# Kernel optimization log

Hardware: AMD Instinct MI355X
Metric: run time of the kernel (lower is better)

The kernel has to match this reference:

```python
import jax, jax.numpy as jnp
import numpy as np
import math

FACTOR = 5

def setup_inputs() -> dict:
    key = jax.random.key(0)
    k1, k2, k3, k4 = jax.random.split(key, 4)
    B, L, H, D = 4, 2048, 8, 64
    sample_k = FACTOR * math.ceil(math.log(L))  # 40
    queries = jax.random.normal(k1, (B, L, H, D), dtype=jnp.float32)
    keys = jax.random.normal(k2, (B, L, H, D), dtype=jnp.float32)
    values = jax.random.normal(k3, (B, L, H, D), dtype=jnp.float32)
    index_sample = jax.random.randint(k4, (L, sample_k), 0, L, dtype=jnp.int32)
    return {"queries": queries, "keys": keys, "values": values, "index_sample": index_sample}

def reference(queries, keys, values, index_sample):
    B, L_Q, H, D = queries.shape
    L_K = keys.shape[1]
    # [B,L,H,D] -> [B,H,L,D]
    Q = jnp.swapaxes(queries, 1, 2)
    K = jnp.swapaxes(keys, 1, 2)
    # values are cumsum'ed along the length axis before attention
    Vc = jnp.cumsum(jnp.swapaxes(values, 1, 2), axis=-2)
    u = min(FACTOR * math.ceil(math.log(L_Q)), L_Q)  # n_top
    # --- _prob_QK ---
    # gather sampled keys per query position: [B,H,L_Q,sample_k,D]
    K_sample = K[:, :, index_sample, :]
    # sampled scores: [B,H,L_Q,sample_k]
    Q_K_sample = jnp.einsum('bhqd,bhqsd->bhqs', Q, K_sample)
    # sparsity measure M = max - mean(scaled by L_K)
    M = Q_K_sample.max(axis=-1) - Q_K_sample.sum(axis=-1) / L_K  # [B,H,L_Q]
    M_top = jax.lax.top_k(M, u)[1]  # [B,H,u] query indices
    # gather top queries: [B,H,u,D]
    Q_reduce = jnp.take_along_axis(Q, M_top[..., None], axis=2)
    # full scores for selected queries: [B,H,u,L_K]
    scores = jnp.einsum('bhud,bhkd->bhuk', Q_reduce, K)
    scale = 1.0 / math.sqrt(D)
    scores = scores * scale
    # mask_flag=False, output_attention=False -> plain softmax then matmul with cumsum'ed V
    attn = jax.nn.softmax(scores, axis=-1)
    context = jnp.einsum('bhuk,bhkd->bhud', attn, Vc)  # [B,H,u,D]
    return context
```

## Files before the change

### kernel.cpp

```cpp
#include <hip/hip_runtime.h>
#include <math.h>

#define B 4
#define L 2048
#define H 8
#define D 64
#define SK 40
#define U 40
#define JC 16
#define JCL (L / JC)
#define CSG 32

#define OFF_M     0
#define OFF_TOP   262144
#define OFF_T     270336
#define OFF_PART  10756096
#define OFF_CSUM  15998976

__device__ __forceinline__ float dot4(float4 a, float4 b) {
    return fmaf(a.x, b.x, fmaf(a.y, b.y, fmaf(a.z, b.z, a.w * b.w)));
}

__global__ __launch_bounds__(256) void k_msamp(const float* __restrict__ Q,
                                               const float* __restrict__ K,
                                               const int* __restrict__ idx,
                                               float* __restrict__ M) {
    int g  = blockIdx.x & 7;
    int b  = g >> 1;
    int hh = g & 1;
    int t  = threadIdx.x;
    int wave = t >> 6;
    int lane = t & 63;
    int qp = lane >> 5;
    int hp = (lane >> 3) & 3;
    int c  = lane & 7;
    int h  = hh * 4 + hp;
    int q  = (blockIdx.x >> 3) * 8 + wave * 2 + qp;

    const float* qrow = Q + (size_t)((b * L + q) * H + h) * D + c * 8;
    float4 qa = *(const float4*)qrow;
    float4 qb = *(const float4*)(qrow + 4);

    int s1 = lane & 31;
    int v1 = idx[q * SK + s1];
    int s2 = 32 + s1; if (s2 > SK - 1) s2 = SK - 1;
    int v2 = idx[q * SK + s2];

    const float* kbase = K + (size_t)b * L * H * D + (size_t)h * D + c * 8;

    float vmax = -__builtin_inff();
    float vsum = 0.f;
#pragma unroll 8
    for (int s = 0; s < SK; ++s) {
        int kidx = (s < 32) ? __shfl(v1, qp * 32 + s, 64)
                            : __shfl(v2, qp * 32 + (s - 32), 64);
        const float* kp = kbase + (size_t)kidx * (H * D);
        float4 ka = *(const float4*)kp;
        float4 kb = *(const float4*)(kp + 4);
        float d8 = dot4(qa, ka) + dot4(qb, kb);
        d8 += __shfl_xor(d8, 1, 64);
        d8 += __shfl_xor(d8, 2, 64);
        d8 += __shfl_xor(d8, 4, 64);
        vmax = fmaxf(vmax, d8);
        vsum += d8;
    }
    if (c == 0) M[(size_t)(b * H + h) * L + q] = vmax - vsum * (1.0f / (float)L);
}

__global__ __launch_bounds__(256) void k_topk(const float* __restrict__ M,
                                              int* __restrict__ top) {
    __shared__ unsigned long long cand[L];
    __shared__ unsigned int bins[256];
    __shared__ unsigned int red[256];
    __shared__ int cnt2;

    int bh = blockIdx.x;
    int tid = threadIdx.x;
    const float* m = M + (size_t)bh * L;

    bins[tid] = 0;
    if (tid == 0) cnt2 = 0;

    const float4* m4 = (const float4*)(m + tid * 8);
    float4 fa = m4[0], fb = m4[1];
    float f8[8] = {fa.x, fa.y, fa.z, fa.w, fb.x, fb.y, fb.z, fb.w};
    unsigned int u8[8];
    unsigned int umin = 0xFFFFFFFFu, umax = 0u;
#pragma unroll
    for (int e = 0; e < 8; ++e) {
        unsigned int bits = __float_as_uint(f8[e]);
        unsigned int u = (bits & 0x80000000u) ? ~bits : (bits | 0x80000000u);
        u8[e] = u;
        umin = min(umin, u);
        umax = max(umax, u);
    }
    red[tid] = umin;
    __syncthreads();
    for (int s = 128; s; s >>= 1) {
        if (tid < s) red[tid] = min(red[tid], red[tid + s]);
        __syncthreads();
    }
    unsigned int kmin = red[0];
    __syncthreads();
    red[tid] = umax;
    __syncthreads();
    for (int s = 128; s; s >>= 1) {
        if (tid < s) red[tid] = max(red[tid], red[tid + s]);
        __syncthreads();
    }
    unsigned int kmax = red[0];
    __syncthreads();

    unsigned int range = kmax - kmin;
    if (range == 0u) {
        if (tid < U) top[bh * U + tid] = tid;
        return;
    }
    int hb = 31 - __clz(range);
    int shift = (hb > 7) ? (hb - 7) : 0;

#pragma unroll
    for (int e = 0; e < 8; ++e) {
        unsigned int bin = (u8[e] - kmin) >> shift;
        atomicAdd(&bins[bin], 1u);
    }
    __syncthreads();

    red[tid] = bins[tid];
    __syncthreads();
    for (int s = 1; s < 256; s <<= 1) {
        unsigned int add = (tid + s < 256) ? red[tid + s] : 0u;
        __syncthreads();
        red[tid] += add;
        __syncthreads();
    }
    int cnt = __syncthreads_count(red[tid] >= U);
    unsigned int t = (unsigned int)(cnt - 1);

#pragma unroll
    for (int e = 0; e < 8; ++e) {
        unsigned int u = u8[e];
        if (((u - kmin) >> shift) >= t) {
            int pos = atomicAdd(&cnt2, 1);
            int i = tid * 8 + e;
            cand[pos] = ((unsigned long long)u << 11) | (unsigned long long)(2047 - i);
        }
    }
    __syncthreads();
    int C = cnt2;

    for (int j = tid; j < C; j += 256) {
        unsigned long long kj = cand[j];
        int r = 0;
        for (int kk = 0; kk < C; ++kk) r += (cand[kk] > kj);
        if (r < U) top[bh * U + r] = 2047 - (int)(kj & 0x7FFull);
    }
}


__global__ __launch_bounds__(512, 4) void k_phA(const float* __restrict__ Q,
                                                const float* __restrict__ K,
                                                const int* __restrict__ top,
                                                float* __restrict__ T,
                                                float* __restrict__ csum) {
    __shared__ __align__(16) float4 sQ4[U * 16];
    int tid = threadIdx.x;
    int bh = blockIdx.x >> 4;
    int kc = blockIdx.x & 15;
    int b = bh >> 3, h = bh & (H - 1);

    for (int i = tid; i < U * 16; i += 512) {
        int u = i >> 4, c = i & 15;
        int qidx = top[bh * U + u];
        sQ4[i] = *((const float4*)(Q + (size_t)((b * L + qidx) * H + h) * D) + c);
    }

    int ugrp   = tid >> 7;
    int colgrp = tid & 127;
    int col = kc * 128 + colgrp;

    const float4* kr = (const float4*)(K + (size_t)((b * L + col) * H + h) * D);
    float4 kv[16];
#pragma unroll
    for (int i = 0; i < 16; ++i) kv[i] = kr[i];
    __syncthreads();

    float* Tb = T + (size_t)bh * U * L;
    int cs = 2 * kc + (colgrp >> 6);
#pragma unroll
    for (int uu = 0; uu < 10; ++uu) {
        int u = ugrp * 10 + uu;
        float s = 0.f;
#pragma unroll
        for (int i = 0; i < 16; ++i) s += dot4(sQ4[u * 16 + i], kv[i]);
        float e = __expf(s * 0.125f);
        Tb[(size_t)u * L + col] = e;
        float c0 = e;
#pragma unroll
        for (int o = 1; o < 64; o <<= 1) c0 += __shfl_xor(c0, o, 64);
        if ((colgrp & 63) == 0) csum[((size_t)bh * U + u) * CSG + cs] = c0;
    }
}

__global__ __launch_bounds__(512, 4) void k_phB(const float* __restrict__ V,
                                                const float* __restrict__ T,
                                                const float* __restrict__ csum,
                                                float* __restrict__ part) {
    __shared__ __align__(16) float sT[U * JCL];
    int tid = threadIdx.x;
    int bh = blockIdx.x >> 4;
    int jc = blockIdx.x & 15;
    int b = bh >> 3, h = bh & (H - 1);
    int w8   = tid >> 6;
    int lane = tid & 63;

    int j2 = lane >> 4;
    int d4 = lane & 15;
    int jlane = lane & 31;

    const float* Eg = T + (size_t)bh * U * L + jc * JCL;
    for (int r = 0; r < 5; ++r) {
        int u = w8 * 5 + r;
        float cv = csum[((size_t)bh * U + u) * CSG + jlane];
        float tv = (jlane > 2 * jc + 1) ? cv : 0.f;
        tv += __shfl_xor(tv, 1, 64);
        tv += __shfl_xor(tv, 2, 64);
        tv += __shfl_xor(tv, 4, 64);
        tv += __shfl_xor(tv, 8, 64);
        tv += __shfl_xor(tv, 16, 64);
        float el = Eg[(size_t)u * L + lane];
        float eh = Eg[(size_t)u * L + 64 + lane];
        float sh = eh;
#pragma unroll
        for (int s = 1; s < 64; s <<= 1) {
            float o = __shfl_down(sh, s, 64);
            sh += (lane + s < 64) ? o : 0.f;
        }
        float th = __shfl(sh, 0, 64);
        float sl = el;
#pragma unroll
        for (int s = 1; s < 64; s <<= 1) {
            float o = __shfl_down(sl, s, 64);
            sl += (lane + s < 64) ? o : 0.f;
        }
        sT[u * JCL + lane]      = sl + th + tv;
        sT[u * JCL + 64 + lane] = sh + tv;
    }
    __syncthreads();

    float4 acc[5];
#pragma unroll
    for (int uu = 0; uu < 5; ++uu) acc[uu] = make_float4(0.f, 0.f, 0.f, 0.f);

    const float* Vb = V + (size_t)(b * L) * (H * D) + (size_t)h * D + d4 * 4;
#pragma unroll 4
    for (int it = 0; it < JCL / 4; ++it) {
        int j = it * 4 + j2;
        float4 v4 = *(const float4*)(Vb + (size_t)(jc * JCL + j) * (H * D));
#pragma unroll
        for (int uu = 0; uu < 5; ++uu) {
            float tj = sT[(w8 * 5 + uu) * JCL + j];
            acc[uu].x = fmaf(tj, v4.x, acc[uu].x);
            acc[uu].y = fmaf(tj, v4.y, acc[uu].y);
            acc[uu].z = fmaf(tj, v4.z, acc[uu].z);
            acc[uu].w = fmaf(tj, v4.w, acc[uu].w);
        }
    }

    float* po = part + ((size_t)jc * (B * H) + bh) * (U * D);
#pragma unroll
    for (int uu = 0; uu < 5; ++uu) {
        float4 a = acc[uu];
        a.x += __shfl_xor(a.x, 16, 64); a.y += __shfl_xor(a.y, 16, 64);
        a.z += __shfl_xor(a.z, 16, 64); a.w += __shfl_xor(a.w, 16, 64);
        a.x += __shfl_xor(a.x, 32, 64); a.y += __shfl_xor(a.y, 32, 64);
        a.z += __shfl_xor(a.z, 32, 64); a.w += __shfl_xor(a.w, 32, 64);
        if (j2 == 0) *(float4*)(po + (w8 * 5 + uu) * D + d4 * 4) = a;
    }
}

__global__ __launch_bounds__(256) void k_red(const float* __restrict__ part,
                                             const float* __restrict__ csum,
                                             float* __restrict__ out) {
    __shared__ float sden[4];
    int o = blockIdx.x * 256 + threadIdx.x;
    int bh = o / (U * D);
    int rest = o - bh * (U * D);
    int u = rest >> 6;
    int tid = threadIdx.x;
    int ubase = ((blockIdx.x * 256) % (U * D)) >> 6;

    if (tid < 128) {
        int ul = tid >> 5, j = tid & 31;
        float v = csum[((size_t)bh * U + ubase + ul) * CSG + j];
        v += __shfl_xor(v, 1, 64);
        v += __shfl_xor(v, 2, 64);
        v += __shfl_xor(v, 4, 64);
        v += __shfl_xor(v, 8, 64);
        v += __shfl_xor(v, 16, 64);
        if (j == 0) sden[ul] = v;
    }
    __syncthreads();

    float s = 0.f;
#pragma unroll
    for (int jc = 0; jc < JC; ++jc)
        s += part[(size_t)(jc * (B * H) + bh) * (U * D) + rest];
    out[o] = s / sden[u - ubase];
}

extern "C" void kernel_launch(void* const* d_in, const int* in_sizes, int n_in,
                              void* d_out, int out_size, void* d_ws, size_t ws_size,
                              hipStream_t stream) {
    const float* Q  = (const float*)d_in[0];
    const float* K  = (const float*)d_in[1];
    const float* V  = (const float*)d_in[2];
    const int* idx  = (const int*)d_in[3];
    float* out = (float*)d_out;

    float* M    = (float*)((char*)d_ws + OFF_M);
    int*   top  = (int*)  ((char*)d_ws + OFF_TOP);
    float* T    = (float*)((char*)d_ws + OFF_T);
    float* part = (float*)((char*)d_ws + OFF_PART);
    float* csum = (float*)((char*)d_ws + OFF_CSUM);

    k_msamp<<<(L / 8) * 8, 256, 0, stream>>>(Q, K, idx, M);
    k_topk<<<B * H, 256, 0, stream>>>(M, top);
    k_phA<<<B * H * 16, 512, 0, stream>>>(Q, K, top, T, csum);
    k_phB<<<B * H * 16, 512, 0, stream>>>(V, T, csum, part);
    k_red<<<(B * H * U * D) / 256, 256, 0, stream>>>(part, csum, out);
}
```

Before: 144.0 us.

## Fuse score and cumsum-V phases, defer cross-chunk prefix to reduction via V sums

Merges the exp-score kernel and the suffix-weighted V accumulation into one kernel, so exponentiated scores stay in shared memory and are never written to or read back from a global T buffer. The cross-chunk suffix term, which needed every chunk's csum before phase B could start, is now applied in the reduction kernel as a weighted sum of per-chunk V column sums. This removes one launch and roughly 10 MB of global traffic. In exchange it adds a vsum buffer, a segmented scan in k_red, and extra LDS use per block (sE of U*JCL floats plus sQ4), which may lower occupancy.

```diff
diff --git a/kernel.cpp b/kernel.cpp
--- a/kernel.cpp
+++ b/kernel.cpp
@@ -13,9 +13,9 @@
 
 #define OFF_M     0
 #define OFF_TOP   262144
-#define OFF_T     270336
-#define OFF_PART  10756096
-#define OFF_CSUM  15998976
+#define OFF_PART  270336
+#define OFF_CSUM  5513216
+#define OFF_VSUM  5677056
 
 __device__ __forceinline__ float dot4(float4 a, float4 b) {
     return fmaf(a.x, b.x, fmaf(a.y, b.y, fmaf(a.z, b.z, a.w * b.w)));
@@ -157,16 +157,18 @@
     }
 }
 
-
-__global__ __launch_bounds__(512, 4) void k_phA(const float* __restrict__ Q,
-                                                const float* __restrict__ K,
-                                                const int* __restrict__ top,
-                                                float* __restrict__ T,
-                                                float* __restrict__ csum) {
+__global__ __launch_bounds__(512, 4) void k_phAB(const float* __restrict__ Q,
+                                                 const float* __restrict__ K,
+                                                 const int* __restrict__ top,
+                                                 const float* __restrict__ V,
+                                                 float* __restrict__ part,
+                                                 float* __restrict__ csum,
+                                                 float* __restrict__ vsum) {
     __shared__ __align__(16) float4 sQ4[U * 16];
+    __shared__ __align__(16) float sE[U * JCL];
     int tid = threadIdx.x;
     int bh = blockIdx.x >> 4;
-    int kc = blockIdx.x & 15;
+    int jc = blockIdx.x & 15;
     int b = bh >> 3, h = bh & (H - 1);
 
     for (int i = tid; i < U * 16; i += 512) {
@@ -177,7 +179,7 @@
 
     int ugrp   = tid >> 7;
     int colgrp = tid & 127;
-    int col = kc * 128 + colgrp;
+    int col = jc * 128 + colgrp;
 
     const float4* kr = (const float4*)(K + (size_t)((b * L + col) * H + h) * D);
     float4 kv[16];
@@ -185,8 +187,7 @@
     for (int i = 0; i < 16; ++i) kv[i] = kr[i];
     __syncthreads();
 
-    float* Tb = T + (size_t)bh * U * L;
-    int cs = 2 * kc + (colgrp >> 6);
+    int cs = 2 * jc + (colgrp >> 6);
 #pragma unroll
     for (int uu = 0; uu < 10; ++uu) {
         int u = ugrp * 10 + uu;
@@ -194,42 +195,20 @@
 #pragma unroll
         for (int i = 0; i < 16; ++i) s += dot4(sQ4[u * 16 + i], kv[i]);
         float e = __expf(s * 0.125f);
-        Tb[(size_t)u * L + col] = e;
+        sE[u * JCL + colgrp] = e;
         float c0 = e;
 #pragma unroll
         for (int o = 1; o < 64; o <<= 1) c0 += __shfl_xor(c0, o, 64);
         if ((colgrp & 63) == 0) csum[((size_t)bh * U + u) * CSG + cs] = c0;
     }
-}
-
-__global__ __launch_bounds__(512, 4) void k_phB(const float* __restrict__ V,
-                                                const float* __restrict__ T,
-                                                const float* __restrict__ csum,
-                                                float* __restrict__ part) {
-    __shared__ __align__(16) float sT[U * JCL];
-    int tid = threadIdx.x;
-    int bh = blockIdx.x >> 4;
-    int jc = blockIdx.x & 15;
-    int b = bh >> 3, h = bh & (H - 1);
+    __syncthreads();
+
     int w8   = tid >> 6;
     int lane = tid & 63;
-
-    int j2 = lane >> 4;
-    int d4 = lane & 15;
-    int jlane = lane & 31;
-
-    const float* Eg = T + (size_t)bh * U * L + jc * JCL;
     for (int r = 0; r < 5; ++r) {
         int u = w8 * 5 + r;
-        float cv = csum[((size_t)bh * U + u) * CSG + jlane];
-        float tv = (jlane > 2 * jc + 1) ? cv : 0.f;
-        tv += __shfl_xor(tv, 1, 64);
-        tv += __shfl_xor(tv, 2, 64);
-        tv += __shfl_xor(tv, 4, 64);
-        tv += __shfl_xor(tv, 8, 64);
-        tv += __shfl_xor(tv, 16, 64);
-        float el = Eg[(size_t)u * L + lane];
-        float eh = Eg[(size_t)u * L + 64 + lane];
+        float el = sE[u * JCL + lane];
+        float eh = sE[u * JCL + 64 + lane];
         float sh = eh;
 #pragma unroll
         for (int s = 1; s < 64; s <<= 1) {
@@ -243,23 +222,27 @@
             float o = __shfl_down(sl, s, 64);
             sl += (lane + s < 64) ? o : 0.f;
         }
-        sT[u * JCL + lane]      = sl + th + tv;
-        sT[u * JCL + 64 + lane] = sh + tv;
-    }
-    __syncthreads();
+        sE[u * JCL + lane]      = sl + th;
+        sE[u * JCL + 64 + lane] = sh;
+    }
+
+    int j2 = lane >> 4;
+    int d4 = lane & 15;
 
     float4 acc[5];
 #pragma unroll
     for (int uu = 0; uu < 5; ++uu) acc[uu] = make_float4(0.f, 0.f, 0.f, 0.f);
+    float4 vs = make_float4(0.f, 0.f, 0.f, 0.f);
 
     const float* Vb = V + (size_t)(b * L) * (H * D) + (size_t)h * D + d4 * 4;
 #pragma unroll 4
     for (int it = 0; it < JCL / 4; ++it) {
         int j = it * 4 + j2;
         float4 v4 = *(const float4*)(Vb + (size_t)(jc * JCL + j) * (H * D));
+        vs.x += v4.x; vs.y += v4.y; vs.z += v4.z; vs.w += v4.w;
 #pragma unroll
         for (int uu = 0; uu < 5; ++uu) {
-            float tj = sT[(w8 * 5 + uu) * JCL + j];
+            float tj = sE[(w8 * 5 + uu) * JCL + j];
             acc[uu].x = fmaf(tj, v4.x, acc[uu].x);
             acc[uu].y = fmaf(tj, v4.y, acc[uu].y);
             acc[uu].z = fmaf(tj, v4.z, acc[uu].z);
@@ -277,36 +260,52 @@
         a.z += __shfl_xor(a.z, 32, 64); a.w += __shfl_xor(a.w, 32, 64);
         if (j2 == 0) *(float4*)(po + (w8 * 5 + uu) * D + d4 * 4) = a;
     }
+    if (w8 == 0) {
+        vs.x += __shfl_xor(vs.x, 16, 64); vs.y += __shfl_xor(vs.y, 16, 64);
+        vs.z += __shfl_xor(vs.z, 16, 64); vs.w += __shfl_xor(vs.w, 16, 64);
+        vs.x += __shfl_xor(vs.x, 32, 64); vs.y += __shfl_xor(vs.y, 32, 64);
+        vs.z += __shfl_xor(vs.z, 32, 64); vs.w += __shfl_xor(vs.w, 32, 64);
+        if (j2 == 0)
+            *(float4*)(vsum + ((size_t)bh * JC + jc) * D + d4 * 4) = vs;
+    }
 }
 
 __global__ __launch_bounds__(256) void k_red(const float* __restrict__ part,
                                              const float* __restrict__ csum,
+                                             const float* __restrict__ vsum,
                                              float* __restrict__ out) {
     __shared__ float sden[4];
+    __shared__ float stw[4][JC];
     int o = blockIdx.x * 256 + threadIdx.x;
     int bh = o / (U * D);
     int rest = o - bh * (U * D);
     int u = rest >> 6;
+    int d = rest & 63;
     int tid = threadIdx.x;
     int ubase = ((blockIdx.x * 256) % (U * D)) >> 6;
 
     if (tid < 128) {
-        int ul = tid >> 5, j = tid & 31;
-        float v = csum[((size_t)bh * U + ubase + ul) * CSG + j];
-        v += __shfl_xor(v, 1, 64);
-        v += __shfl_xor(v, 2, 64);
-        v += __shfl_xor(v, 4, 64);
-        v += __shfl_xor(v, 8, 64);
-        v += __shfl_xor(v, 16, 64);
-        if (j == 0) sden[ul] = v;
-    }
-    __syncthreads();
-
+        int ul = tid >> 5, cs = tid & 31;
+        float v = csum[((size_t)bh * U + ubase + ul) * CSG + cs];
+#pragma unroll
+        for (int s = 1; s < 32; s <<= 1) {
+            float ov = __shfl_down(v, s, 64);
+            v += (cs + s < 32) ? ov : 0.f;
+        }
+        if (cs == 0) { sden[ul] = v; stw[ul][JC - 1] = 0.f; }
+        if ((cs & 1) == 0 && cs >= 2) stw[ul][(cs >> 1) - 1] = v;
+    }
+    __syncthreads();
+
+    int ul = u - ubase;
     float s = 0.f;
 #pragma unroll
     for (int jc = 0; jc < JC; ++jc)
         s += part[(size_t)(jc * (B * H) + bh) * (U * D) + rest];
-    out[o] = s / sden[u - ubase];
+#pragma unroll
+    for (int jc = 0; jc < JC; ++jc)
+        s = fmaf(stw[ul][jc], vsum[((size_t)bh * JC + jc) * D + d], s);
+    out[o] = s / sden[ul];
 }
 
 extern "C" void kernel_launch(void* const* d_in, const int* in_sizes, int n_in,
@@ -320,13 +319,12 @@
 
     float* M    = (float*)((char*)d_ws + OFF_M);
     int*   top  = (int*)  ((char*)d_ws + OFF_TOP);
-    float* T    = (float*)((char*)d_ws + OFF_T);
     float* part = (float*)((char*)d_ws + OFF_PART);
     float* csum = (float*)((char*)d_ws + OFF_CSUM);
+    float* vsum = (float*)((char*)d_ws + OFF_VSUM);
 
     k_msamp<<<(L / 8) * 8, 256, 0, stream>>>(Q, K, idx, M);
     k_topk<<<B * H, 256, 0, stream>>>(M, top);
-    k_phA<<<B * H * 16, 512, 0, stream>>>(Q, K, top, T, csum);
-    k_phB<<<B * H * 16, 512, 0, stream>>>(V, T, csum, part);
-    k_red<<<(B * H * U * D) / 256, 256, 0, stream>>>(part, csum, out);
-}
+    k_phAB<<<B * H * JC, 512, 0, stream>>>(Q, K, top, V, part, csum, vsum);
+    k_red<<<(B * H * U * D) / 256, 256, 0, stream>>>(part, csum, vsum, out);
+}
```

Result: faster. 140.1 us (median of 2 runs) (-2.7%).
